# Optimization experiments

Measured on AMD Instinct MI355X. Metric: run time of the kernel, lower is better.

## Reference

```python
import jax, jax.numpy as jnp
import numpy as np

EMBED_DIM = 1024
NUM_HEADS = 16
HEAD_DIM = EMBED_DIM // NUM_HEADS
CHUNK_SIZE = 10
LEFT_CONTEXT = 25
RIGHT_CONTEXT = 0
NEG_INF = -1e30  # stands in for float('-inf') additive mask, safe under softmax


def chunk_attention_mask(seq_len: int) -> jnp.ndarray:
    """Vectorized version of the per-row Python loop mask builder.
    Row i may attend to: its own chunk [chunk_start, chunk_end), the left
    context [i-left_context, chunk_start), and the right context
    [chunk_end, i+right_context+1)."""
    i = jnp.arange(seq_len)[:, None]
    j = jnp.arange(seq_len)[None, :]
    chunk_start = (i // CHUNK_SIZE) * CHUNK_SIZE
    chunk_end = jnp.minimum(chunk_start + CHUNK_SIZE, seq_len)
    in_chunk = (j >= chunk_start) & (j < chunk_end)
    in_left = (j >= i - LEFT_CONTEXT) & (j < chunk_start)
    in_right = (j >= chunk_end) & (j < jnp.minimum(seq_len, i + RIGHT_CONTEXT + 1))
    allowed = in_chunk | in_left | in_right
    return jnp.where(allowed, 0.0, NEG_INF).astype(jnp.float32)


def setup_inputs() -> dict:
    key = jax.random.key(0)
    ks = jax.random.split(key, 9)
    B, S, E = 2, 2048, EMBED_DIM
    s = 1.0 / np.sqrt(E)
    return {
        "hidden_states": jax.random.normal(ks[0], (B, S, E), jnp.float32),
        "Wq": jax.random.normal(ks[1], (E, E), jnp.float32) * s,
        "bq": jax.random.normal(ks[2], (E,), jnp.float32) * 0.02,
        "Wk": jax.random.normal(ks[3], (E, E), jnp.float32) * s,
        "bk": jax.random.normal(ks[4], (E,), jnp.float32) * 0.02,
        "Wv": jax.random.normal(ks[5], (E, E), jnp.float32) * s,
        "bv": jax.random.normal(ks[6], (E,), jnp.float32) * 0.02,
        "Wo": jax.random.normal(ks[7], (E, E), jnp.float32) * s,
        "bo": jax.random.normal(ks[8], (E,), jnp.float32) * 0.02,
    }


def reference(hidden_states, Wq, bq, Wk, bk, Wv, bv, Wo, bo):
    B, S, E = hidden_states.shape
    H, D = NUM_HEADS, HEAD_DIM
    scaling = D ** -0.5

    def proj(x, W, b):  # nn.Linear: x @ W.T + b, then split heads -> [B,H,S,D]
        y = jnp.einsum('bse,fe->bsf', x, W) + b
        return y.reshape(B, S, H, D).transpose(0, 2, 1, 3)

    q = proj(hidden_states, Wq, bq) * scaling
    k = proj(hidden_states, Wk, bk)
    v = proj(hidden_states, Wv, bv)

    scores = jnp.einsum('bhsd,bhtd->bhst', q, k)  # [B,H,S,S]
    scores = scores + chunk_attention_mask(S)[None, None]
    probs = jax.nn.softmax(scores, axis=-1)
    out = jnp.einsum('bhst,bhtd->bhsd', probs, v)  # [B,H,S,D]
    out = out.transpose(0, 2, 1, 3).reshape(B, S, E)
    out = jnp.einsum('bse,fe->bsf', out, Wo) + bo
    return out
```

## Files before the change

### kernel.cpp

```cpp
#include <hip/hip_runtime.h>
#include <stdint.h>

typedef unsigned short u16;
typedef __attribute__((ext_vector_type(8))) short short8;
typedef __attribute__((ext_vector_type(4))) short short4v;
typedef __attribute__((ext_vector_type(4))) float f32x4;

#define AS1 __attribute__((address_space(1)))
#define AS3 __attribute__((address_space(3)))

__device__ __forceinline__ u16 f2bf(float f) {
  uint32_t x = __builtin_bit_cast(uint32_t, f);
  uint32_t r = (x + 0x7fffu + ((x >> 16) & 1u)) >> 16;
  return (u16)r;
}
__device__ __forceinline__ float bf2f(u16 u) {
  return __builtin_bit_cast(float, (uint32_t)u << 16);
}

__device__ __forceinline__ void conv8(const float* __restrict__ s, u16* __restrict__ d, float sc) {
  float4 a = *(const float4*)s;
  float4 b = *(const float4*)(s + 4);
  union { u16 u[8]; uint4 v; } pk;
  pk.u[0] = f2bf(a.x * sc); pk.u[1] = f2bf(a.y * sc); pk.u[2] = f2bf(a.z * sc); pk.u[3] = f2bf(a.w * sc);
  pk.u[4] = f2bf(b.x * sc); pk.u[5] = f2bf(b.y * sc); pk.u[6] = f2bf(b.z * sc); pk.u[7] = f2bf(b.w * sc);
  *(uint4*)d = pk.v;
}
__device__ __forceinline__ void copy8f(const float* __restrict__ s, float* __restrict__ d, float sc) {
  float4 a = *(const float4*)s;
  float4 b = *(const float4*)(s + 4);
  a.x *= sc; a.y *= sc; a.z *= sc; a.w *= sc;
  b.x *= sc; b.y *= sc; b.z *= sc; b.w *= sc;
  *(float4*)d = a; *(float4*)(d + 4) = b;
}

__global__ void pack_kernel(const float* __restrict__ X,
                            const float* __restrict__ Wq, const float* __restrict__ bq,
                            const float* __restrict__ Wk, const float* __restrict__ bk,
                            const float* __restrict__ Wv, const float* __restrict__ bv,
                            const float* __restrict__ Wo,
                            u16* __restrict__ Xbf, u16* __restrict__ Wcat,
                            u16* __restrict__ Wobf, float* __restrict__ bcat) {
  int t = blockIdx.x * blockDim.x + threadIdx.x;
  if (t < 524288) { conv8(X + (size_t)t * 8, Xbf + (size_t)t * 8, 1.f); return; }
  t -= 524288;
  if (t < 131072) { conv8(Wq + (size_t)t * 8, Wcat + (size_t)t * 8, 0.125f); return; }
  t -= 131072;
  if (t < 131072) { conv8(Wk + (size_t)t * 8, Wcat + 1048576 + (size_t)t * 8, 1.f); return; }
  t -= 131072;
  if (t < 131072) { conv8(Wv + (size_t)t * 8, Wcat + 2097152 + (size_t)t * 8, 1.f); return; }
  t -= 131072;
  if (t < 131072) { conv8(Wo + (size_t)t * 8, Wobf + (size_t)t * 8, 1.f); return; }
  t -= 131072;
  if (t < 128) { copy8f(bq + t * 8, bcat + t * 8, 0.125f); return; }
  t -= 128;
  if (t < 128) { copy8f(bk + t * 8, bcat + 1024 + t * 8, 1.f); return; }
  t -= 128;
  if (t < 128) { copy8f(bv + t * 8, bcat + 2048 + t * 8, 1.f); return; }
}

template <int BN, bool OUT_BF16>
__global__ __launch_bounds__(512)
void gemm_bt(const u16* __restrict__ A, const u16* __restrict__ Bt,
             const float* __restrict__ bias, u16* __restrict__ Cbf,
             float* __restrict__ Cf, int M, int N, int K) {
  constexpr int SEG_A = 8;
  constexpr int SEG_B = BN / 16;
  constexpr int NSEG = SEG_A + SEG_B;
  constexpr int NWN = BN / 32;
  constexpr int NWM = 8 / NWN;
  constexpr int MI = 128 / (NWM * 16);
  __shared__ u16 As[2][128 * 32];
  __shared__ u16 Bs[2][BN * 32];
  const int wv = threadIdx.x >> 6;
  const int lane = threadIdx.x & 63;
  const int bm = blockIdx.x, bn = blockIdx.y;
  const int wm = wv / NWN, wn = wv % NWN;
  const int lrow = lane & 15, quad = lane >> 4;

  f32x4 acc[MI][2];
#pragma unroll
  for (int i = 0; i < MI; ++i)
#pragma unroll
    for (int j = 0; j < 2; ++j) acc[i][j] = (f32x4){0.f, 0.f, 0.f, 0.f};

  const long arow = (long)bm * 128;
  const long brow = (long)bn * BN;
  const int srow = lane >> 2;
  const int scol = ((lane & 3) ^ ((lane >> 3) & 3)) * 8;
  const int swz = (quad ^ ((lrow >> 1) & 3)) * 8;

  auto stage = [&](int nb, int k0) {
#pragma unroll
    for (int it = 0; it < 2; ++it) {
      const int s = wv + it * 8;
      if (s < NSEG) {
        const u16* g;
        u16* l;
        if (s < SEG_A) {
          g = A + (arow + s * 16 + srow) * K + k0 + scol;
          l = (u16*)As[nb] + s * 512;
        } else {
          g = Bt + (brow + (s - SEG_A) * 16 + srow) * K + k0 + scol;
          l = (u16*)Bs[nb] + (s - SEG_A) * 512;
        }
        __builtin_amdgcn_global_load_lds((AS1 void*)g, (AS3 void*)l, 16, 0, 0);
      }
    }
  };

  stage(0, 0);
  int cur = 0;
  for (int k0 = 0; k0 < K; k0 += 32) {
    __syncthreads();
    if (k0 + 32 < K) stage(cur ^ 1, k0 + 32);

    short8 af[MI], bfr[2];
#pragma unroll
    for (int mi = 0; mi < MI; ++mi)
      af[mi] = *(const short8*)(As[cur] + (wm * (MI * 16) + mi * 16 + lrow) * 32 + swz);
#pragma unroll
    for (int ni = 0; ni < 2; ++ni)
      bfr[ni] = *(const short8*)(Bs[cur] + (wn * 32 + ni * 16 + lrow) * 32 + swz);
#pragma unroll
    for (int mi = 0; mi < MI; ++mi)
#pragma unroll
      for (int ni = 0; ni < 2; ++ni)
        acc[mi][ni] = __builtin_amdgcn_mfma_f32_16x16x32_bf16(af[mi], bfr[ni], acc[mi][ni], 0, 0, 0);
    cur ^= 1;
  }

#pragma unroll
  for (int mi = 0; mi < MI; ++mi) {
#pragma unroll
    for (int ni = 0; ni < 2; ++ni) {
      const int col = bn * BN + wn * 32 + ni * 16 + lrow;
      const float bv = bias[col];
#pragma unroll
      for (int r = 0; r < 4; ++r) {
        const int row = bm * 128 + wm * (MI * 16) + mi * 16 + quad * 4 + r;
        const float v = acc[mi][ni][r] + bv;
        if constexpr (OUT_BF16) Cbf[(long)row * N + col] = f2bf(v);
        else Cf[(long)row * N + col] = v;
      }
    }
  }
}

#define NCH 205
#define VT_STRIDE 68
#define PB_STRIDE 72
#define WAVE_LDS (64 * VT_STRIDE + 16 * PB_STRIDE)

__global__ __launch_bounds__(256)
void attn_kernel(const u16* __restrict__ QKV, u16* __restrict__ ctx) {
  __shared__ __align__(16) u16 lds[4 * WAVE_LDS];
  const int wv = threadIdx.x >> 6;
  const int lane = threadIdx.x & 63;
  u16* Vt = lds + wv * WAVE_LDS;
  u16* Pb = Vt + 64 * VT_STRIDE;

  const int n = lane & 15, quad = lane >> 4;

  const int gw = blockIdx.x * 4 + wv;
  const int b = gw / (16 * NCH);
  int rem = gw - b * 16 * NCH;
  const int h = rem / NCH;
  const int c = rem - h * NCH;
  const int cs = c * 10;
  const int nq = min(10, 2048 - cs);
  const int w0 = max(cs - 25, 0);
  const int L = cs + nq - w0;

  const long base = ((long)b * 2048) * 3072 + (long)h * 64;

  for (int idx = lane; idx < (64 * VT_STRIDE) / 8; idx += 64)
    *(uint4*)(Vt + idx * 8) = (uint4){0, 0, 0, 0};
  for (int idx = lane; idx < (16 * PB_STRIDE) / 8; idx += 64)
    *(uint4*)(Pb + idx * 8) = (uint4){0, 0, 0, 0};

  for (int j = 0; j < L; ++j)
    Vt[lane * VT_STRIDE + j] = QKV[base + (long)(w0 + j) * 3072 + 2048 + lane];

  const int mclamp = min(n, nq - 1);
  const long qrow = base + (long)(cs + mclamp) * 3072;
  short8 aq0 = *(const short8*)(QKV + qrow + quad * 8);
  short8 aq1 = *(const short8*)(QKV + qrow + 32 + quad * 8);

  f32x4 sc[3];
#pragma unroll
  for (int t = 0; t < 3; ++t) {
    const int jj = min(16 * t + n, L - 1);
    const long krow = base + (long)(w0 + jj) * 3072 + 1024;
    short8 bk0 = *(const short8*)(QKV + krow + quad * 8);
    short8 bk1 = *(const short8*)(QKV + krow + 32 + quad * 8);
    f32x4 z = (f32x4){0.f, 0.f, 0.f, 0.f};
    z = __builtin_amdgcn_mfma_f32_16x16x32_bf16(aq0, bk0, z, 0, 0, 0);
    sc[t] = __builtin_amdgcn_mfma_f32_16x16x32_bf16(aq1, bk1, z, 0, 0, 0);
  }

#pragma unroll
  for (int r = 0; r < 4; ++r) {
    const int i = cs + quad * 4 + r;
    const int jlo = max(i - 25, 0) - w0;
    float v0 = (n >= jlo && n < L)      ? sc[0][r] : -1e30f;
    float v1 = (16 + n >= jlo && 16 + n < L) ? sc[1][r] : -1e30f;
    float v2 = (32 + n >= jlo && 32 + n < L) ? sc[2][r] : -1e30f;
    float m = fmaxf(v0, fmaxf(v1, v2));
#pragma unroll
    for (int off = 8; off > 0; off >>= 1) m = fmaxf(m, __shfl_xor(m, off));
    float p0 = __expf(v0 - m), p1 = __expf(v1 - m), p2 = __expf(v2 - m);
    float sum = p0 + p1 + p2;
#pragma unroll
    for (int off = 8; off > 0; off >>= 1) sum += __shfl_xor(sum, off);
    const float inv = 1.f / sum;
    u16* prow = Pb + (quad * 4 + r) * PB_STRIDE;
    prow[n]      = f2bf(p0 * inv);
    prow[16 + n] = f2bf(p1 * inv);
    prow[32 + n] = f2bf(p2 * inv);
  }

  short8 ap0 = *(const short8*)(Pb + n * PB_STRIDE + quad * 8);
  short8 ap1 = *(const short8*)(Pb + n * PB_STRIDE + 32 + quad * 8);
  f32x4 o[4];
#pragma unroll
  for (int dt = 0; dt < 4; ++dt) {
    const u16* vrow = Vt + (dt * 16 + n) * VT_STRIDE;
    short4v l0 = *(const short4v*)(vrow + quad * 8);
    short4v h0 = *(const short4v*)(vrow + quad * 8 + 4);
    short4v l1 = *(const short4v*)(vrow + 32 + quad * 8);
    short4v h1 = *(const short4v*)(vrow + 32 + quad * 8 + 4);
    short8 bv0 = __builtin_shufflevector(l0, h0, 0, 1, 2, 3, 4, 5, 6, 7);
    short8 bv1 = __builtin_shufflevector(l1, h1, 0, 1, 2, 3, 4, 5, 6, 7);
    f32x4 z = (f32x4){0.f, 0.f, 0.f, 0.f};
    z = __builtin_amdgcn_mfma_f32_16x16x32_bf16(ap0, bv0, z, 0, 0, 0);
    o[dt] = __builtin_amdgcn_mfma_f32_16x16x32_bf16(ap1, bv1, z, 0, 0, 0);
  }

#pragma unroll
  for (int dt = 0; dt < 4; ++dt) {
#pragma unroll
    for (int r = 0; r < 4; ++r) {
      const int row = quad * 4 + r;
      if (row < nq)
        ctx[((long)b * 2048 + cs + row) * 1024 + h * 64 + dt * 16 + n] = f2bf(o[dt][r]);
    }
  }
}

extern "C" void kernel_launch(void* const* d_in, const int* in_sizes, int n_in,
                              void* d_out, int out_size, void* d_ws, size_t ws_size,
                              hipStream_t stream) {
  const float* X  = (const float*)d_in[0];
  const float* Wq = (const float*)d_in[1];
  const float* bq = (const float*)d_in[2];
  const float* Wk = (const float*)d_in[3];
  const float* bk = (const float*)d_in[4];
  const float* Wv = (const float*)d_in[5];
  const float* bv = (const float*)d_in[6];
  const float* Wo = (const float*)d_in[7];
  const float* bo = (const float*)d_in[8];
  float* out = (float*)d_out;

  char* ws = (char*)d_ws;
  u16* Xbf   = (u16*)(ws);
  u16* Wcat  = (u16*)(ws + 8388608);
  u16* Wobf  = (u16*)(ws + 14680064);
  float* bcat = (float*)(ws + 16777216);
  u16* QKV   = (u16*)(ws + 16789504);
  u16* ctx   = (u16*)(ws + 41955328);

  pack_kernel<<<4098, 256, 0, stream>>>(X, Wq, bq, Wk, bk, Wv, bv, Wo, Xbf, Wcat, Wobf, bcat);
  gemm_bt<128, true ><<<dim3(32, 24), 512, 0, stream>>>(Xbf, Wcat, bcat, QKV, nullptr, 4096, 3072, 1024);
  attn_kernel<<<1640, 256, 0, stream>>>(QKV, ctx);
  gemm_bt<64, false><<<dim3(32, 16), 512, 0, stream>>>(ctx, Wobf, bo, nullptr, out, 4096, 1024, 1024);
}
```

Measured before the change: 162.5 us.

## Stage V row-major with vectorized loads and gather columns for PV MFMA

The attention kernel now copies the V window into LDS in its natural row-major layout using 16-byte global loads spread across lanes, instead of a per-key scalar transpose loop. This also drops the zeroing of the V buffer and shrinks its LDS footprint. The PV MFMA operands are built by 8 scalar LDS reads per fragment, with row indices clamped to the last valid key so no padding is needed. The aim is to cut the serialized, uncoalesced global V loads, at the cost of more LDS reads per MFMA operand.

Result: faster. 157.5 us, median of 2 (-3.1%).

```diff
diff --git a/kernel.cpp b/kernel.cpp
--- a/kernel.cpp
+++ b/kernel.cpp
@@ -148,17 +148,17 @@
 }
 
 #define NCH 205
-#define VT_STRIDE 68
+#define VR_STRIDE 68
 #define PB_STRIDE 72
-#define WAVE_LDS (64 * VT_STRIDE + 16 * PB_STRIDE)
+#define WAVE_LDS (36 * VR_STRIDE + 16 * PB_STRIDE)
 
 __global__ __launch_bounds__(256)
 void attn_kernel(const u16* __restrict__ QKV, u16* __restrict__ ctx) {
   __shared__ __align__(16) u16 lds[4 * WAVE_LDS];
   const int wv = threadIdx.x >> 6;
   const int lane = threadIdx.x & 63;
-  u16* Vt = lds + wv * WAVE_LDS;
-  u16* Pb = Vt + 64 * VT_STRIDE;
+  u16* Vr = lds + wv * WAVE_LDS;
+  u16* Pb = Vr + 36 * VR_STRIDE;
 
   const int n = lane & 15, quad = lane >> 4;
 
@@ -174,13 +174,20 @@
 
   const long base = ((long)b * 2048) * 3072 + (long)h * 64;
 
-  for (int idx = lane; idx < (64 * VT_STRIDE) / 8; idx += 64)
-    *(uint4*)(Vt + idx * 8) = (uint4){0, 0, 0, 0};
   for (int idx = lane; idx < (16 * PB_STRIDE) / 8; idx += 64)
     *(uint4*)(Pb + idx * 8) = (uint4){0, 0, 0, 0};
 
-  for (int j = 0; j < L; ++j)
-    Vt[lane * VT_STRIDE + j] = QKV[base + (long)(w0 + j) * 3072 + 2048 + lane];
+#pragma unroll
+  for (int it = 0; it < 5; ++it) {
+    const int slot = it * 64 + lane;
+    const int j = slot >> 3, c8 = slot & 7;
+    if (j < L) {
+      const uint4 v = *(const uint4*)(QKV + base + (long)(w0 + j) * 3072 + 2048 + c8 * 8);
+      u16* wp = Vr + j * VR_STRIDE + c8 * 8;
+      *(uint2*)wp = (uint2){v.x, v.y};
+      *(uint2*)(wp + 4) = (uint2){v.z, v.w};
+    }
+  }
 
   const int mclamp = min(n, nq - 1);
   const long qrow = base + (long)(cs + mclamp) * 3072;
@@ -222,16 +229,21 @@
 
   short8 ap0 = *(const short8*)(Pb + n * PB_STRIDE + quad * 8);
   short8 ap1 = *(const short8*)(Pb + n * PB_STRIDE + 32 + quad * 8);
+  const int icap = (L - 1) * VR_STRIDE;
+  const int ib0 = (quad * 8) * VR_STRIDE;
+  const int ib1 = ib0 + 32 * VR_STRIDE;
   f32x4 o[4];
 #pragma unroll
   for (int dt = 0; dt < 4; ++dt) {
-    const u16* vrow = Vt + (dt * 16 + n) * VT_STRIDE;
-    short4v l0 = *(const short4v*)(vrow + quad * 8);
-    short4v h0 = *(const short4v*)(vrow + quad * 8 + 4);
-    short4v l1 = *(const short4v*)(vrow + 32 + quad * 8);
-    short4v h1 = *(const short4v*)(vrow + 32 + quad * 8 + 4);
-    short8 bv0 = __builtin_shufflevector(l0, h0, 0, 1, 2, 3, 4, 5, 6, 7);
-    short8 bv1 = __builtin_shufflevector(l1, h1, 0, 1, 2, 3, 4, 5, 6, 7);
+    const u16* colp = Vr + dt * 16 + n;
+    short8 bv0, bv1;
+#pragma unroll
+    for (int e = 0; e < 8; ++e) {
+      int i0 = ib0 + e * VR_STRIDE; i0 = i0 < icap ? i0 : icap;
+      int i1 = ib1 + e * VR_STRIDE; i1 = i1 < icap ? i1 : icap;
+      bv0[e] = (short)colp[i0];
+      bv1[e] = (short)colp[i1];
+    }
     f32x4 z = (f32x4){0.f, 0.f, 0.f, 0.f};
     z = __builtin_amdgcn_mfma_f32_16x16x32_bf16(ap0, bv0, z, 0, 0, 0);
     o[dt] = __builtin_amdgcn_mfma_f32_16x16x32_bf16(ap1, bv1, z, 0, 0, 0);
```
